# Optimization experiments

Measured on AMD Instinct MI355X. Metric: run time of the kernel, lower is better.

## Reference

```python
import jax, jax.numpy as jnp
import numpy as np

B, L, D, H = 2, 2048, 1024, 16
NEG = -1.0e9


def setup_inputs() -> dict:
    key = jax.random.key(0)
    k1, k2, k3, k4 = jax.random.split(key, 4)
    query = jax.random.normal(k1, (B, L, D), dtype=jnp.float32)
    key_t = jax.random.normal(k2, (B, L, D), dtype=jnp.float32)
    value = jax.random.normal(k3, (B, L, D), dtype=jnp.float32)
    # Conv1D c_proj params: w ~ N(0, 0.02), b = 0   (nx=D -> nf=D)
    w_proj = 0.02 * jax.random.normal(k4, (D, D), dtype=jnp.float32)
    b_proj = jnp.zeros((D,), dtype=jnp.float32)
    return {"query": query, "key": key_t, "value": value,
            "w_proj": w_proj, "b_proj": b_proj, "n_head": H}


def reference(query, key, value, w_proj, b_proj, n_head):
    b, l, d = query.shape
    dh = d // n_head
    # split_heads -> [B, H, L, dh]
    q = query.reshape(b, l, n_head, dh).transpose(0, 2, 1, 3)
    k = key.reshape(b, l, n_head, dh).transpose(0, 2, 1, 3)
    v = value.reshape(b, l, n_head, dh).transpose(0, 2, 1, 3)
    # scores: [B, H, L, L], scaled by sqrt(head_dim) (v.size(-1) after split)
    w = jnp.einsum("bhqd,bhkd->bhqk", q, k) / jnp.sqrt(jnp.float32(dh))
    # one_dir_visible=True: multiplicative causal mask, w*m + (-1e9)*(1-m)
    m = jnp.tril(jnp.ones((l, l), dtype=w.dtype))[None, None]
    w = w * m + NEG * (1.0 - m)
    p = jax.nn.softmax(w, axis=-1)  # attn_dropout p=0 -> identity
    a = jnp.einsum("bhqk,bhkd->bhqd", p, v)  # [B, H, L, dh]
    # merge_heads -> [B, L, D]
    a = a.transpose(0, 2, 1, 3).reshape(b, l, d)
    # c_proj (Conv1D == dense): resid_dropout p=0 -> identity
    return a @ w_proj + b_proj
```

## Files before the change

### kernel.cpp

```cpp
#include <hip/hip_runtime.h>
#include <hip/hip_bf16.h>

constexpr int kB  = 2;
constexpr int kL  = 2048;
constexpr int kD  = 1024;
constexpr int kH  = 16;
constexpr int kDH = 64;
constexpr int kM  = kB * kL;

typedef _Float16 half8 __attribute__((ext_vector_type(8)));
typedef _Float16 half4 __attribute__((ext_vector_type(4)));
typedef float    f32x4 __attribute__((ext_vector_type(4)));
typedef unsigned int uint4v __attribute__((ext_vector_type(4)));

constexpr size_t kKhOff = 0;
constexpr size_t kVtOff = 8388608;
constexpr size_t kAhOff = 16777216;
constexpr size_t kWtOff = 25165824;
constexpr size_t kWsNeed = 27262976;

__device__ __forceinline__ void load16_lds(const void* g, void* l) {
    __builtin_amdgcn_global_load_lds((__attribute__((address_space(1))) void*)(g),
                                     (__attribute__((address_space(3))) void*)(l),
                                     16, 0, 0);
}

__global__ __launch_bounds__(256) void conv_fused(const float* __restrict__ K,
                                                  const float* __restrict__ V,
                                                  const float* __restrict__ W,
                                                  _Float16* __restrict__ Kh,
                                                  _Float16* __restrict__ Vt,
                                                  _Float16* __restrict__ Wt) {
    __shared__ _Float16 Ts[64][68];
    const int t = threadIdx.x;
    const int bid = blockIdx.x;

    if (bid < 2048) {
        size_t i = ((size_t)bid * 256 + t) * 8;
        float4 f0 = *(const float4*)(K + i);
        float4 f1 = *(const float4*)(K + i + 4);
        half8 h;
        h[0] = (_Float16)f0.x; h[1] = (_Float16)f0.y; h[2] = (_Float16)f0.z; h[3] = (_Float16)f0.w;
        h[4] = (_Float16)f1.x; h[5] = (_Float16)f1.y; h[6] = (_Float16)f1.z; h[7] = (_Float16)f1.w;
        *(half8*)(Kh + i) = h;
        return;
    }

    const float* src;      size_t src_stride;
    _Float16* dst;         size_t dst_stride;
    if (bid < 3072) {
        const int b2 = bid - 2048;
        const int lt = b2 & 31, h = (b2 >> 5) & 15, b = b2 >> 9;
        src = V + ((size_t)(b * kL + lt * 64)) * kD + h * kDH;
        src_stride = kD;
        dst = Vt + ((size_t)(b * kH + h) * kDH) * kL + lt * 64;
        dst_stride = kL;
    } else {
        const int b3 = bid - 3072;
        const int nt = b3 & 15, kt = b3 >> 4;
        src = W + (size_t)(kt * 64) * kD + nt * 64;
        src_stride = kD;
        dst = Wt + (size_t)(nt * 64) * kD + kt * 64;
        dst_stride = kD;
    }

    #pragma unroll
    for (int p = 0; p < 4; ++p) {
        int idx = p * 1024 + t * 4;
        int r = idx >> 6, c = idx & 63;
        float4 f = *(const float4*)(src + (size_t)r * src_stride + c);
        half4 h;
        h[0] = (_Float16)f.x; h[1] = (_Float16)f.y; h[2] = (_Float16)f.z; h[3] = (_Float16)f.w;
        *(half4*)&Ts[r][c] = h;
    }
    __syncthreads();
    #pragma unroll
    for (int p = 0; p < 4; ++p) {
        int idx = p * 1024 + t * 4;
        int ch = idx >> 6, l0 = idx & 63;
        half4 h;
        h[0] = Ts[l0 + 0][ch]; h[1] = Ts[l0 + 1][ch];
        h[2] = Ts[l0 + 2][ch]; h[3] = Ts[l0 + 3][ch];
        *(half4*)(dst + (size_t)ch * dst_stride + l0) = h;
    }
}

__global__ __launch_bounds__(256, 4) void flash_kernel(const float* __restrict__ Q,
                                                       const _Float16* __restrict__ Kh,
                                                       const _Float16* __restrict__ Vt,
                                                       _Float16* __restrict__ Ah) {
    __shared__ __align__(16) _Float16 Ks[2][64 * 64];
    __shared__ __align__(16) _Float16 Vs[2][64 * 64];

    const int t = threadIdx.x;
    const int lane = t & 63, w = t >> 6;
    const int l15 = lane & 15, quad = lane >> 4;

    const int bp32 = ((lane ^ 32) << 2);
    const int bp16 = ((lane ^ 16) << 2);

    const int bid = blockIdx.x;
    const int bh = bid & 31;
    const int p  = bid >> 5;
    const int b = bh >> 4, h = bh & 15;
    const size_t hoff = (size_t)h * kDH;

    const int srow = w * 16 + (lane >> 3);
    const int sj   = ((lane & 7) - (lane >> 3)) & 7;
    const _Float16* kgp = Kh + (size_t)(b * kL) * kD + hoff + sj * 8;
    const _Float16* vgp = Vt + (size_t)(bh * kDH) * kL + sj * 8;

    half8 ones;
    #pragma unroll
    for (int i = 0; i < 8; ++i) ones[i] = (_Float16)1.0f;

    for (int ph = 0; ph < 2; ++ph) {
        const int qt = ph ? (31 - p) : p;
        const int Tq = qt + 1;
        const int qrow0 = qt * 64 + w * 16;

        half8 aq[2];
        #pragma unroll
        for (int kc = 0; kc < 2; ++kc) {
            const float* qp = Q + (size_t)(b * kL + qrow0 + l15) * kD + hoff + kc * 32 + quad * 8;
            float4 f0 = *(const float4*)qp;
            float4 f1 = *(const float4*)(qp + 4);
            half8 hq;
            hq[0] = (_Float16)(f0.x * 0.125f); hq[1] = (_Float16)(f0.y * 0.125f);
            hq[2] = (_Float16)(f0.z * 0.125f); hq[3] = (_Float16)(f0.w * 0.125f);
            hq[4] = (_Float16)(f1.x * 0.125f); hq[5] = (_Float16)(f1.y * 0.125f);
            hq[6] = (_Float16)(f1.z * 0.125f); hq[7] = (_Float16)(f1.w * 0.125f);
            aq[kc] = hq;
        }

        f32x4 o[4];
        f32x4 lsum = (f32x4){0.f, 0.f, 0.f, 0.f};
        #pragma unroll
        for (int nt = 0; nt < 4; ++nt) o[nt] = (f32x4){0.f, 0.f, 0.f, 0.f};

        load16_lds(kgp + (size_t)srow * kD,       &Ks[0][(w * 16) * 64]);
        load16_lds(kgp + (size_t)(srow + 8) * kD, &Ks[0][(w * 16 + 8) * 64]);
        load16_lds(vgp + (size_t)srow * kL,       &Vs[0][(w * 16) * 64]);
        load16_lds(vgp + (size_t)(srow + 8) * kL, &Vs[0][(w * 16 + 8) * 64]);

        for (int kt = 0; kt < Tq; ++kt) {
            const int cur = kt & 1;
            const int kb = kt * 64;
            __syncthreads();

            if (kt + 1 < Tq) {
                const int kb1 = kb + 64;
                load16_lds(kgp + (size_t)(kb1 + srow) * kD,     &Ks[cur ^ 1][(w * 16) * 64]);
                load16_lds(kgp + (size_t)(kb1 + srow + 8) * kD, &Ks[cur ^ 1][(w * 16 + 8) * 64]);
                load16_lds(vgp + (size_t)srow * kL + kb1,       &Vs[cur ^ 1][(w * 16) * 64]);
                load16_lds(vgp + (size_t)(srow + 8) * kL + kb1, &Vs[cur ^ 1][(w * 16 + 8) * 64]);
            }

            f32x4 sT[4];
            #pragma unroll
            for (int nt = 0; nt < 4; ++nt) {
                sT[nt] = (f32x4){0.f, 0.f, 0.f, 0.f};
                #pragma unroll
                for (int kc = 0; kc < 2; ++kc) {
                    const int r = nt * 16 + l15;
                    const int slot = (quad + 4 * kc + l15) & 7;
                    half8 bk = *(half8*)&Ks[cur][r * 64 + slot * 8];
                    sT[nt] = __builtin_amdgcn_mfma_f32_16x16x32_f16(bk, aq[kc], sT[nt], 0, 0, 0);
                }
            }

            if (kt == Tq - 1) {
                const int qa = qrow0 + l15;
                const int keyb = kb + quad * 4;
                #pragma unroll
                for (int nt = 0; nt < 4; ++nt)
                    #pragma unroll
                    for (int r = 0; r < 4; ++r)
                        if (keyb + nt * 16 + r > qa) sT[nt][r] = -1.0e30f;
            }

            uint32_t pk0[4], pk1[4];
            #pragma unroll
            for (int nt = 0; nt < 4; ++nt) {
                float e0 = __expf(sT[nt][0] - 8.0f);
                float e1 = __expf(sT[nt][1] - 8.0f);
                float e2 = __expf(sT[nt][2] - 8.0f);
                float e3 = __expf(sT[nt][3] - 8.0f);
                auto h01 = __builtin_amdgcn_cvt_pkrtz(e0, e1);
                auto h23 = __builtin_amdgcn_cvt_pkrtz(e2, e3);
                pk0[nt] = __builtin_bit_cast(uint32_t, h01);
                pk1[nt] = __builtin_bit_cast(uint32_t, h23);
            }

            uint32_t lo[2][2], hi[2][2];
            #pragma unroll
            for (int a = 0; a < 2; ++a)
                #pragma unroll
                for (int d = 0; d < 2; ++d) {
                    const uint32_t pe = d ? pk1[2 * a]     : pk0[2 * a];
                    const uint32_t po = d ? pk1[2 * a + 1] : pk0[2 * a + 1];
                    const uint32_t send1 = (quad < 2) ? po : pe;
                    const uint32_t own   = (quad < 2) ? pe : po;
                    const uint32_t recv  =
                        (uint32_t)__builtin_amdgcn_ds_bpermute(bp32, (int)send1);
                    const bool k03 = (quad == 0) || (quad == 3);
                    const uint32_t send2 = k03 ? recv : own;
                    const uint32_t kept  = k03 ? own : recv;
                    const uint32_t got   =
                        (uint32_t)__builtin_amdgcn_ds_bpermute(bp16, (int)send2);
                    lo[a][d] = (quad & 1) ? got : kept;
                    hi[a][d] = (quad & 1) ? kept : got;
                }

            half8 ap[2];
            #pragma unroll
            for (int kc = 0; kc < 2; ++kc) {
                uint4v u = (uint4v){lo[kc][0], lo[kc][1], hi[kc][0], hi[kc][1]};
                ap[kc] = __builtin_bit_cast(half8, u);
            }

            #pragma unroll
            for (int nt = 0; nt < 4; ++nt)
                #pragma unroll
                for (int kc = 0; kc < 2; ++kc) {
                    const int r = nt * 16 + l15;
                    const int slot = (quad + 4 * kc + l15) & 7;
                    half8 bv = *(half8*)&Vs[cur][r * 64 + slot * 8];
                    o[nt] = __builtin_amdgcn_mfma_f32_16x16x32_f16(ap[kc], bv, o[nt], 0, 0, 0);
                }
            lsum = __builtin_amdgcn_mfma_f32_16x16x32_f16(ap[0], ones, lsum, 0, 0, 0);
            lsum = __builtin_amdgcn_mfma_f32_16x16x32_f16(ap[1], ones, lsum, 0, 0, 0);
        }

        const size_t orow = (size_t)(b * kL + qrow0 + quad * 4);
        #pragma unroll
        for (int r = 0; r < 4; ++r) {
            float inv = 1.0f / lsum[r];
            #pragma unroll
            for (int nt = 0; nt < 4; ++nt)
                Ah[(orow + r) * kD + hoff + nt * 16 + l15] = (_Float16)(o[nt][r] * inv);
        }

        __syncthreads();
    }
}

__global__ __launch_bounds__(256, 2) void proj_half(const _Float16* __restrict__ Ah,
                                                    const _Float16* __restrict__ Wt,
                                                    const float* __restrict__ bias,
                                                    float* __restrict__ out) {
    __shared__ __align__(16) _Float16 As[2][128 * 64];
    __shared__ __align__(16) _Float16 Bs[2][64 * 64];

    const int t = threadIdx.x;
    const int lane = t & 63, w = t >> 6;
    const int l15 = lane & 15, quad = lane >> 4;
    const int m0 = blockIdx.x * 128, n0 = blockIdx.y * 64;

    const int srowA = w * 32 + (lane >> 3);
    const int srowB = w * 16 + (lane >> 3);
    const int sj    = ((lane & 7) - (lane >> 3)) & 7;
    const _Float16* agp = Ah + (size_t)(m0 + srowA) * kD + sj * 8;
    const _Float16* bgp = Wt + (size_t)(n0 + srowB) * kD + sj * 8;

    auto stage = [&](int buf, int k1) {
        load16_lds(agp + (size_t) 0 * kD + k1, &As[buf][(w * 32 +  0) * 64]);
        load16_lds(agp + (size_t) 8 * kD + k1, &As[buf][(w * 32 +  8) * 64]);
        load16_lds(agp + (size_t)16 * kD + k1, &As[buf][(w * 32 + 16) * 64]);
        load16_lds(agp + (size_t)24 * kD + k1, &As[buf][(w * 32 + 24) * 64]);
        load16_lds(bgp + (size_t) 0 * kD + k1, &Bs[buf][(w * 16 +  0) * 64]);
        load16_lds(bgp + (size_t) 8 * kD + k1, &Bs[buf][(w * 16 +  8) * 64]);
    };

    f32x4 c[2][4];
    #pragma unroll
    for (int rg = 0; rg < 2; ++rg)
        #pragma unroll
        for (int nt = 0; nt < 4; ++nt) c[rg][nt] = (f32x4){0.f, 0.f, 0.f, 0.f};

    stage(0, 0);

    for (int kt = 0; kt < 16; ++kt) {
        const int cur = kt & 1;
        __syncthreads();

        if (kt + 1 < 16) stage(cur ^ 1, (kt + 1) * 64);

        #pragma unroll
        for (int kc = 0; kc < 2; ++kc) {
            const int slot = (kc * 4 + quad + l15) & 7;
            half8 a0 = *(half8*)&As[cur][(w * 32 +  0 + l15) * 64 + slot * 8];
            half8 a1 = *(half8*)&As[cur][(w * 32 + 16 + l15) * 64 + slot * 8];
            #pragma unroll
            for (int nt = 0; nt < 4; ++nt) {
                half8 bf = *(half8*)&Bs[cur][(nt * 16 + l15) * 64 + slot * 8];
                c[0][nt] = __builtin_amdgcn_mfma_f32_16x16x32_f16(a0, bf, c[0][nt], 0, 0, 0);
                c[1][nt] = __builtin_amdgcn_mfma_f32_16x16x32_f16(a1, bf, c[1][nt], 0, 0, 0);
            }
        }
    }

    #pragma unroll
    for (int nt = 0; nt < 4; ++nt) {
        const int n = n0 + nt * 16 + l15;
        const float bv = bias[n];
        #pragma unroll
        for (int rg = 0; rg < 2; ++rg) {
            const int mrow = m0 + w * 32 + rg * 16 + quad * 4;
            #pragma unroll
            for (int r = 0; r < 4; ++r)
                out[(size_t)(mrow + r) * kD + n] = c[rg][nt][r] + bv;
        }
    }
}

__global__ __launch_bounds__(256) void attn_kernel_f32(const float* __restrict__ Q,
                                                       const float* __restrict__ K,
                                                       const float* __restrict__ V,
                                                       float* __restrict__ A) {
    const int lane = threadIdx.x & 63;
    const int wave = threadIdx.x >> 6;
    const int tilesPerBH = kL / 4;
    const int bh = blockIdx.x / tilesPerBH;
    const int tile = blockIdx.x % tilesPerBH;
    const int b = bh / kH, h = bh % kH;
    const int qi = tile * 4 + wave;
    const size_t base = (size_t)b * kL * kD + (size_t)h * kDH;
    const float* kptr = K + base;
    const float* vptr = V + base;
    const float qd = Q[base + (size_t)qi * kD + lane] * 0.125f;
    float m = -3.0e38f, l = 0.0f, acc = 0.0f;
    for (int j = 0; j <= qi; ++j) {
        const float kd = kptr[(size_t)j * kD + lane];
        float s = qd * kd;
        #pragma unroll
        for (int off = 32; off; off >>= 1) s += __shfl_xor(s, off);
        const float mnew = fmaxf(m, s);
        const float corr = __expf(m - mnew);
        const float p = __expf(s - mnew);
        const float vd = vptr[(size_t)j * kD + lane];
        l = l * corr + p;
        acc = acc * corr + p * vd;
        m = mnew;
    }
    A[base + (size_t)qi * kD + lane] = acc / l;
}

__global__ __launch_bounds__(256) void proj_kernel_f32(const float* __restrict__ A,
                                                       const float* __restrict__ W,
                                                       const float* __restrict__ bias,
                                                       float* __restrict__ out) {
    __shared__ __align__(16) float As[16][64];
    __shared__ __align__(16) float Ws[16][64];
    const int t = threadIdx.x;
    const int m0 = blockIdx.x * 64, n0 = blockIdx.y * 64;
    const int tx = t & 15, ty = t >> 4;
    const int arow = t >> 2, acol4 = (t & 3) * 4;
    const int wrow = t >> 4, wcol4 = (t & 15) * 4;
    float c[4][4] = {};
    for (int k0 = 0; k0 < kD; k0 += 16) {
        const float4 av = *(const float4*)(A + (size_t)(m0 + arow) * kD + k0 + acol4);
        const float4 wv = *(const float4*)(W + (size_t)(k0 + wrow) * kD + n0 + wcol4);
        __syncthreads();
        As[acol4 + 0][arow] = av.x;
        As[acol4 + 1][arow] = av.y;
        As[acol4 + 2][arow] = av.z;
        As[acol4 + 3][arow] = av.w;
        *(float4*)&Ws[wrow][wcol4] = wv;
        __syncthreads();
        #pragma unroll
        for (int kk = 0; kk < 16; ++kk) {
            const float4 a = *(const float4*)&As[kk][ty * 4];
            const float4 wv2 = *(const float4*)&Ws[kk][tx * 4];
            c[0][0] += a.x * wv2.x; c[0][1] += a.x * wv2.y; c[0][2] += a.x * wv2.z; c[0][3] += a.x * wv2.w;
            c[1][0] += a.y * wv2.x; c[1][1] += a.y * wv2.y; c[1][2] += a.y * wv2.z; c[1][3] += a.y * wv2.w;
            c[2][0] += a.z * wv2.x; c[2][1] += a.z * wv2.y; c[2][2] += a.z * wv2.z; c[2][3] += a.z * wv2.w;
            c[3][0] += a.w * wv2.x; c[3][1] += a.w * wv2.y; c[3][2] += a.w * wv2.z; c[3][3] += a.w * wv2.w;
        }
    }
    const float4 bv = *(const float4*)(bias + n0 + tx * 4);
    #pragma unroll
    for (int i = 0; i < 4; ++i) {
        float4 o;
        o.x = c[i][0] + bv.x; o.y = c[i][1] + bv.y; o.z = c[i][2] + bv.z; o.w = c[i][3] + bv.w;
        *(float4*)(out + (size_t)(m0 + ty * 4 + i) * kD + n0 + tx * 4) = o;
    }
}

extern "C" void kernel_launch(void* const* d_in, const int* in_sizes, int n_in,
                              void* d_out, int out_size, void* d_ws, size_t ws_size,
                              hipStream_t stream) {
    const float* Q    = (const float*)d_in[0];
    const float* K    = (const float*)d_in[1];
    const float* V    = (const float*)d_in[2];
    const float* W    = (const float*)d_in[3];
    const float* bias = (const float*)d_in[4];
    float* out = (float*)d_out;

    if (ws_size >= kWsNeed) {
        char* ws = (char*)d_ws;
        _Float16* Kh = (_Float16*)(ws + kKhOff);
        _Float16* Vt = (_Float16*)(ws + kVtOff);
        _Float16* Ah = (_Float16*)(ws + kAhOff);
        _Float16* Wt = (_Float16*)(ws + kWtOff);

        conv_fused<<<dim3(3328), 256, 0, stream>>>(K, V, W, Kh, Vt, Wt);
        flash_kernel<<<dim3(512), 256, 0, stream>>>(Q, Kh, Vt, Ah);
        proj_half<<<dim3(kM / 128, kD / 64), 256, 0, stream>>>(Ah, Wt, bias, out);
    } else {
        float* A = (float*)d_ws;
        attn_kernel_f32<<<dim3(kB * kH * (kL / 4)), 256, 0, stream>>>(Q, K, V, A);
        proj_kernel_f32<<<dim3(kM / 64, kD / 64), 256, 0, stream>>>(A, W, bias, out);
    }
}
```

Before: 154.5 us.

## Process both paired query tiles in one key sweep to share K/V loads

Instead of running the low and high query tiles of each block as two sequential phases, the kernel now iterates over key tiles once (up to the high tile) and computes both query tiles against each staged K/V tile, skipping the low tile once past its diagonal. This roughly halves K/V global-to-LDS traffic and barrier count for the short phase, and overlaps the two tiles' MFMA/exp work. It doubles accumulator and score registers per thread, which may raise register pressure and hurt occupancy under the 4-waves launch bound.

```diff
diff --git a/kernel.cpp b/kernel.cpp
--- a/kernel.cpp
+++ b/kernel.cpp
@@ -102,6 +102,7 @@
     const int bid = blockIdx.x;
     const int bh = bid & 31;
     const int p  = bid >> 5;
+    const int qtLo = p, qtHi = 31 - p;
     const int b = bh >> 4, h = bh & 15;
     const size_t hoff = (size_t)h * kDH;
 
@@ -114,15 +115,15 @@
     #pragma unroll
     for (int i = 0; i < 8; ++i) ones[i] = (_Float16)1.0f;
 
-    for (int ph = 0; ph < 2; ++ph) {
-        const int qt = ph ? (31 - p) : p;
-        const int Tq = qt + 1;
-        const int qrow0 = qt * 64 + w * 16;
-
-        half8 aq[2];
-        #pragma unroll
-        for (int kc = 0; kc < 2; ++kc) {
-            const float* qp = Q + (size_t)(b * kL + qrow0 + l15) * kD + hoff + kc * 32 + quad * 8;
+    const int qrow0Lo = qtLo * 64 + w * 16;
+    const int qrow0Hi = qtHi * 64 + w * 16;
+    half8 aqLo[2], aqHi[2];
+    #pragma unroll
+    for (int kc = 0; kc < 2; ++kc) {
+        #pragma unroll
+        for (int g = 0; g < 2; ++g) {
+            const int qr = g ? qrow0Hi : qrow0Lo;
+            const float* qp = Q + (size_t)(b * kL + qr + l15) * kD + hoff + kc * 32 + quad * 8;
             float4 f0 = *(const float4*)qp;
             float4 f1 = *(const float4*)(qp + 4);
             half8 hq;
@@ -130,118 +131,154 @@
             hq[2] = (_Float16)(f0.z * 0.125f); hq[3] = (_Float16)(f0.w * 0.125f);
             hq[4] = (_Float16)(f1.x * 0.125f); hq[5] = (_Float16)(f1.y * 0.125f);
             hq[6] = (_Float16)(f1.z * 0.125f); hq[7] = (_Float16)(f1.w * 0.125f);
-            aq[kc] = hq;
-        }
-
-        f32x4 o[4];
-        f32x4 lsum = (f32x4){0.f, 0.f, 0.f, 0.f};
-        #pragma unroll
-        for (int nt = 0; nt < 4; ++nt) o[nt] = (f32x4){0.f, 0.f, 0.f, 0.f};
-
-        load16_lds(kgp + (size_t)srow * kD,       &Ks[0][(w * 16) * 64]);
-        load16_lds(kgp + (size_t)(srow + 8) * kD, &Ks[0][(w * 16 + 8) * 64]);
-        load16_lds(vgp + (size_t)srow * kL,       &Vs[0][(w * 16) * 64]);
-        load16_lds(vgp + (size_t)(srow + 8) * kL, &Vs[0][(w * 16 + 8) * 64]);
-
-        for (int kt = 0; kt < Tq; ++kt) {
-            const int cur = kt & 1;
-            const int kb = kt * 64;
-            __syncthreads();
-
-            if (kt + 1 < Tq) {
-                const int kb1 = kb + 64;
-                load16_lds(kgp + (size_t)(kb1 + srow) * kD,     &Ks[cur ^ 1][(w * 16) * 64]);
-                load16_lds(kgp + (size_t)(kb1 + srow + 8) * kD, &Ks[cur ^ 1][(w * 16 + 8) * 64]);
-                load16_lds(vgp + (size_t)srow * kL + kb1,       &Vs[cur ^ 1][(w * 16) * 64]);
-                load16_lds(vgp + (size_t)(srow + 8) * kL + kb1, &Vs[cur ^ 1][(w * 16 + 8) * 64]);
+            if (g) aqHi[kc] = hq; else aqLo[kc] = hq;
+        }
+    }
+
+    f32x4 oLo[4], oHi[4];
+    f32x4 lsumLo = (f32x4){0.f, 0.f, 0.f, 0.f};
+    f32x4 lsumHi = (f32x4){0.f, 0.f, 0.f, 0.f};
+    #pragma unroll
+    for (int nt = 0; nt < 4; ++nt) {
+        oLo[nt] = (f32x4){0.f, 0.f, 0.f, 0.f};
+        oHi[nt] = (f32x4){0.f, 0.f, 0.f, 0.f};
+    }
+
+    auto make_ap = [&](const f32x4* sTg, half8* apg) {
+        uint32_t pk0[4], pk1[4];
+        #pragma unroll
+        for (int nt = 0; nt < 4; ++nt) {
+            float e0 = __expf(sTg[nt][0] - 8.0f);
+            float e1 = __expf(sTg[nt][1] - 8.0f);
+            float e2 = __expf(sTg[nt][2] - 8.0f);
+            float e3 = __expf(sTg[nt][3] - 8.0f);
+            auto h01 = __builtin_amdgcn_cvt_pkrtz(e0, e1);
+            auto h23 = __builtin_amdgcn_cvt_pkrtz(e2, e3);
+            pk0[nt] = __builtin_bit_cast(uint32_t, h01);
+            pk1[nt] = __builtin_bit_cast(uint32_t, h23);
+        }
+        uint32_t blo[2][2], bhi[2][2];
+        #pragma unroll
+        for (int a = 0; a < 2; ++a)
+            #pragma unroll
+            for (int d = 0; d < 2; ++d) {
+                const uint32_t pe = d ? pk1[2 * a]     : pk0[2 * a];
+                const uint32_t po = d ? pk1[2 * a + 1] : pk0[2 * a + 1];
+                const uint32_t send1 = (quad < 2) ? po : pe;
+                const uint32_t own   = (quad < 2) ? pe : po;
+                const uint32_t recv  =
+                    (uint32_t)__builtin_amdgcn_ds_bpermute(bp32, (int)send1);
+                const bool k03 = (quad == 0) || (quad == 3);
+                const uint32_t send2 = k03 ? recv : own;
+                const uint32_t kept  = k03 ? own : recv;
+                const uint32_t got   =
+                    (uint32_t)__builtin_amdgcn_ds_bpermute(bp16, (int)send2);
+                blo[a][d] = (quad & 1) ? got : kept;
+                bhi[a][d] = (quad & 1) ? kept : got;
             }
-
-            f32x4 sT[4];
-            #pragma unroll
-            for (int nt = 0; nt < 4; ++nt) {
-                sT[nt] = (f32x4){0.f, 0.f, 0.f, 0.f};
-                #pragma unroll
-                for (int kc = 0; kc < 2; ++kc) {
-                    const int r = nt * 16 + l15;
-                    const int slot = (quad + 4 * kc + l15) & 7;
-                    half8 bk = *(half8*)&Ks[cur][r * 64 + slot * 8];
-                    sT[nt] = __builtin_amdgcn_mfma_f32_16x16x32_f16(bk, aq[kc], sT[nt], 0, 0, 0);
-                }
+        #pragma unroll
+        for (int kc = 0; kc < 2; ++kc) {
+            uint4v u = (uint4v){blo[kc][0], blo[kc][1], bhi[kc][0], bhi[kc][1]};
+            apg[kc] = __builtin_bit_cast(half8, u);
+        }
+    };
+
+    load16_lds(kgp + (size_t)srow * kD,       &Ks[0][(w * 16) * 64]);
+    load16_lds(kgp + (size_t)(srow + 8) * kD, &Ks[0][(w * 16 + 8) * 64]);
+    load16_lds(vgp + (size_t)srow * kL,       &Vs[0][(w * 16) * 64]);
+    load16_lds(vgp + (size_t)(srow + 8) * kL, &Vs[0][(w * 16 + 8) * 64]);
+
+    for (int kt = 0; kt <= qtHi; ++kt) {
+        const int cur = kt & 1;
+        const int kb = kt * 64;
+        const bool g0on = (kt <= qtLo);
+        __syncthreads();
+
+        if (kt < qtHi) {
+            const int kb1 = kb + 64;
+            load16_lds(kgp + (size_t)(kb1 + srow) * kD,     &Ks[cur ^ 1][(w * 16) * 64]);
+            load16_lds(kgp + (size_t)(kb1 + srow + 8) * kD, &Ks[cur ^ 1][(w * 16 + 8) * 64]);
+            load16_lds(vgp + (size_t)srow * kL + kb1,       &Vs[cur ^ 1][(w * 16) * 64]);
+            load16_lds(vgp + (size_t)(srow + 8) * kL + kb1, &Vs[cur ^ 1][(w * 16 + 8) * 64]);
+        }
+
+        f32x4 sTLo[4], sTHi[4];
+        #pragma unroll
+        for (int nt = 0; nt < 4; ++nt) {
+            sTHi[nt] = (f32x4){0.f, 0.f, 0.f, 0.f};
+            sTLo[nt] = (f32x4){0.f, 0.f, 0.f, 0.f};
+            #pragma unroll
+            for (int kc = 0; kc < 2; ++kc) {
+                const int r = nt * 16 + l15;
+                const int slot = (quad + 4 * kc + l15) & 7;
+                half8 bk = *(half8*)&Ks[cur][r * 64 + slot * 8];
+                sTHi[nt] = __builtin_amdgcn_mfma_f32_16x16x32_f16(bk, aqHi[kc], sTHi[nt], 0, 0, 0);
+                if (g0on)
+                    sTLo[nt] = __builtin_amdgcn_mfma_f32_16x16x32_f16(bk, aqLo[kc], sTLo[nt], 0, 0, 0);
             }
-
-            if (kt == Tq - 1) {
-                const int qa = qrow0 + l15;
-                const int keyb = kb + quad * 4;
-                #pragma unroll
-                for (int nt = 0; nt < 4; ++nt)
-                    #pragma unroll
-                    for (int r = 0; r < 4; ++r)
-                        if (keyb + nt * 16 + r > qa) sT[nt][r] = -1.0e30f;
-            }
-
-            uint32_t pk0[4], pk1[4];
-            #pragma unroll
-            for (int nt = 0; nt < 4; ++nt) {
-                float e0 = __expf(sT[nt][0] - 8.0f);
-                float e1 = __expf(sT[nt][1] - 8.0f);
-                float e2 = __expf(sT[nt][2] - 8.0f);
-                float e3 = __expf(sT[nt][3] - 8.0f);
-                auto h01 = __builtin_amdgcn_cvt_pkrtz(e0, e1);
-                auto h23 = __builtin_amdgcn_cvt_pkrtz(e2, e3);
-                pk0[nt] = __builtin_bit_cast(uint32_t, h01);
-                pk1[nt] = __builtin_bit_cast(uint32_t, h23);
-            }
-
-            uint32_t lo[2][2], hi[2][2];
-            #pragma unroll
-            for (int a = 0; a < 2; ++a)
-                #pragma unroll
-                for (int d = 0; d < 2; ++d) {
-                    const uint32_t pe = d ? pk1[2 * a]     : pk0[2 * a];
-                    const uint32_t po = d ? pk1[2 * a + 1] : pk0[2 * a + 1];
-                    const uint32_t send1 = (quad < 2) ? po : pe;
-                    const uint32_t own   = (quad < 2) ? pe : po;
-                    const uint32_t recv  =
-                        (uint32_t)__builtin_amdgcn_ds_bpermute(bp32, (int)send1);
-                    const bool k03 = (quad == 0) || (quad == 3);
-                    const uint32_t send2 = k03 ? recv : own;
-                    const uint32_t kept  = k03 ? own : recv;
-                    const uint32_t got   =
-                        (uint32_t)__builtin_amdgcn_ds_bpermute(bp16, (int)send2);
-                    lo[a][d] = (quad & 1) ? got : kept;
-                    hi[a][d] = (quad & 1) ? kept : got;
-                }
-
-            half8 ap[2];
-            #pragma unroll
-            for (int kc = 0; kc < 2; ++kc) {
-                uint4v u = (uint4v){lo[kc][0], lo[kc][1], hi[kc][0], hi[kc][1]};
-                ap[kc] = __builtin_bit_cast(half8, u);
-            }
-
+        }
+
+        if (kt == qtHi) {
+            const int qa = qrow0Hi + l15;
+            const int keyb = kb + quad * 4;
             #pragma unroll
             for (int nt = 0; nt < 4; ++nt)
                 #pragma unroll
-                for (int kc = 0; kc < 2; ++kc) {
-                    const int r = nt * 16 + l15;
-                    const int slot = (quad + 4 * kc + l15) & 7;
-                    half8 bv = *(half8*)&Vs[cur][r * 64 + slot * 8];
-                    o[nt] = __builtin_amdgcn_mfma_f32_16x16x32_f16(ap[kc], bv, o[nt], 0, 0, 0);
-                }
-            lsum = __builtin_amdgcn_mfma_f32_16x16x32_f16(ap[0], ones, lsum, 0, 0, 0);
-            lsum = __builtin_amdgcn_mfma_f32_16x16x32_f16(ap[1], ones, lsum, 0, 0, 0);
-        }
-
-        const size_t orow = (size_t)(b * kL + qrow0 + quad * 4);
+                for (int r = 0; r < 4; ++r)
+                    if (keyb + nt * 16 + r > qa) sTHi[nt][r] = -1.0e30f;
+        }
+        if (g0on && kt == qtLo) {
+            const int qa = qrow0Lo + l15;
+            const int keyb = kb + quad * 4;
+            #pragma unroll
+            for (int nt = 0; nt < 4; ++nt)
+                #pragma unroll
+                for (int r = 0; r < 4; ++r)
+                    if (keyb + nt * 16 + r > qa) sTLo[nt][r] = -1.0e30f;
+        }
+
+        half8 apHi[2], apLo[2];
+        make_ap(sTHi, apHi);
+        if (g0on) make_ap(sTLo, apLo);
+
+        #pragma unroll
+        for (int nt = 0; nt < 4; ++nt)
+            #pragma unroll
+            for (int kc = 0; kc < 2; ++kc) {
+                const int r = nt * 16 + l15;
+                const int slot = (quad + 4 * kc + l15) & 7;
+                half8 bv = *(half8*)&Vs[cur][r * 64 + slot * 8];
+                oHi[nt] = __builtin_amdgcn_mfma_f32_16x16x32_f16(apHi[kc], bv, oHi[nt], 0, 0, 0);
+                if (g0on)
+                    oLo[nt] = __builtin_amdgcn_mfma_f32_16x16x32_f16(apLo[kc], bv, oLo[nt], 0, 0, 0);
+            }
+        lsumHi = __builtin_amdgcn_mfma_f32_16x16x32_f16(apHi[0], ones, lsumHi, 0, 0, 0);
+        lsumHi = __builtin_amdgcn_mfma_f32_16x16x32_f16(apHi[1], ones, lsumHi, 0, 0, 0);
+        if (g0on) {
+            lsumLo = __builtin_amdgcn_mfma_f32_16x16x32_f16(apLo[0], ones, lsumLo, 0, 0, 0);
+            lsumLo = __builtin_amdgcn_mfma_f32_16x16x32_f16(apLo[1], ones, lsumLo, 0, 0, 0);
+        }
+    }
+
+    {
+        const size_t orow = (size_t)(b * kL + qrow0Hi + quad * 4);
         #pragma unroll
         for (int r = 0; r < 4; ++r) {
-            float inv = 1.0f / lsum[r];
+            float inv = 1.0f / lsumHi[r];
             #pragma unroll
             for (int nt = 0; nt < 4; ++nt)
-                Ah[(orow + r) * kD + hoff + nt * 16 + l15] = (_Float16)(o[nt][r] * inv);
-        }
-
-        __syncthreads();
+                Ah[(orow + r) * kD + hoff + nt * 16 + l15] = (_Float16)(oHi[nt][r] * inv);
+        }
+    }
+    {
+        const size_t orow = (size_t)(b * kL + qrow0Lo + quad * 4);
+        #pragma unroll
+        for (int r = 0; r < 4; ++r) {
+            float inv = 1.0f / lsumLo[r];
+            #pragma unroll
+            for (int nt = 0; nt < 4; ++nt)
+                Ah[(orow + r) * kD + hoff + nt * 16 + l15] = (_Float16)(oLo[nt][r] * inv);
+        }
     }
 }
 
```

New measurement: 166.7 us. +7.9%, slower.
